# Kernel optimization log

Measured on AMD Instinct MI355X. Metric: run time of the kernel, lower is better.

Reference implementation:

```python
import jax, jax.numpy as jnp
import numpy as np

T, IN, OUT, R = 8192, 4096, 4096, 64


def setup_inputs() -> dict:
    key = jax.random.key(0)
    ks = jax.random.split(key, 7)
    # signed int4 values in [-8, 8) for activations and (unpacked) weights
    quant_x = jax.random.randint(ks[0], (T, IN), -8, 8, dtype=jnp.int32)
    weight_q = jax.random.randint(ks[1], (OUT, IN), -8, 8, dtype=jnp.int32)
    # positive per-token / per-channel symmetric-quant scales
    scale_x = jax.random.uniform(ks[2], (T,), dtype=jnp.float32) * 0.01 + 1e-4
    weight_scales = jax.random.uniform(ks[3], (OUT,), dtype=jnp.float32) * 0.01 + 1e-4
    outlier_x = jax.random.normal(ks[4], (T, R), dtype=jnp.float32)
    w_outlier = jax.random.normal(ks[5], (OUT, R), dtype=jnp.float32)
    bias = jax.random.normal(ks[6], (OUT,), dtype=jnp.float32)
    return {"quant_x": quant_x, "weight_q": weight_q, "scale_x": scale_x,
            "weight_scales": weight_scales, "outlier_x": outlier_x,
            "w_outlier": w_outlier, "bias": bias}


def reference(quant_x, weight_q, scale_x, weight_scales, outlier_x, w_outlier, bias):
    acc = jnp.matmul(quant_x, weight_q.T)
    # sym_dequant: per-row activation scale * per-column weight scale
    x_out = acc.astype(jnp.float32) * scale_x[:, None] * weight_scales[None, :]
    # outlier low-rank addmm + bias epilogue
    x_out = x_out + jnp.matmul(outlier_x, w_outlier.T) + bias
    return x_out
```

## Files before the change

kernel.cpp:

```cpp
#include <hip/hip_runtime.h>

#define T_DIM 8192
#define IN_DIM 4096
#define OUT_DIM 4096
#define R_DIM 64
#define NKP 32

typedef int i32x4 __attribute__((ext_vector_type(4)));
typedef float f32x4 __attribute__((ext_vector_type(4)));
typedef _Float16 f16x8 __attribute__((ext_vector_type(8)));

__device__ __forceinline__ int pack4(int4 v) {
  return (v.x & 255) | ((v.y & 255) << 8) | ((v.z & 255) << 16) | ((unsigned)v.w << 24);
}

__device__ __forceinline__ void gload16(const void* g, void* l) {
  __builtin_amdgcn_global_load_lds(
      (const __attribute__((address_space(1))) void*)(unsigned long long)g,
      (__attribute__((address_space(3))) void*)(unsigned)(unsigned long long)l,
      16, 0, 0);
}

__device__ __forceinline__ i32x4 unp(int x, int y) {
  i32x4 r;
  r[0] = x & 0x0F0F0F0F;
  r[1] = (x >> 4) & 0x0F0F0F0F;
  r[2] = y & 0x0F0F0F0F;
  r[3] = (y >> 4) & 0x0F0F0F0F;
  return r;
}

__device__ __forceinline__ unsigned pb(int a, int b) {
  return (unsigned)(a + 8) | ((unsigned)(b + 8) << 4);
}

__global__ __launch_bounds__(256)
void cvt_pack_kernel(const int* __restrict__ qx, const int* __restrict__ wq,
                     char* __restrict__ pk, int* __restrict__ SS) {
  const int wave = blockIdx.x * 4 + (threadIdx.x >> 6);
  const int l = threadIdx.x & 63;
  const int nw = gridDim.x * 4;
  for (int r = wave; r < T_DIM + OUT_DIM; r += nw) {
    const int* src = (r < T_DIM) ? (qx + (size_t)r * IN_DIM)
                                 : (wq + (size_t)(r - T_DIM) * IN_DIM);
    const int4* src4 = (const int4*)src;
    char* dst = pk + (size_t)r * 2048;
    const int rx = (r >> 1) & 3;
    int s = 0;
#pragma unroll
    for (int i = 0; i < 4; ++i) {
      const int q = i * 64 + l;
      const int kt = q >> 2, g = q & 3;
      int4 s0 = src4[q * 4 + 0], s1 = src4[q * 4 + 1];
      int4 s2 = src4[q * 4 + 2], s3 = src4[q * 4 + 3];
      s += s0.x + s0.y + s0.z + s0.w + s1.x + s1.y + s1.z + s1.w +
           s2.x + s2.y + s2.z + s2.w + s3.x + s3.y + s3.z + s3.w;
      unsigned dw0 = pb(s0.x, s0.y) | (pb(s0.z, s0.w) << 8) |
                     (pb(s1.x, s1.y) << 16) | (pb(s1.z, s1.w) << 24);
      unsigned dw1 = pb(s2.x, s2.y) | (pb(s2.z, s2.w) << 8) |
                     (pb(s3.x, s3.y) << 16) | (pb(s3.z, s3.w) << 24);
      const int off = (kt >> 1) * 64 + ((g ^ rx) << 4) + (kt & 1) * 8;
      *(uint2*)(dst + off) = make_uint2(dw0, dw1);
    }
#pragma unroll
    for (int off = 1; off < 64; off <<= 1) s += __shfl_xor(s, off, 64);
    if (l == 0) SS[r] = s + 8 * IN_DIM;
  }
}

__global__ __launch_bounds__(256, 2)
void w4a4_gemm(const char* __restrict__ A8, const char* __restrict__ B8,
               const int* __restrict__ SS,
               const float* __restrict__ sx, const float* __restrict__ sw,
               const float* __restrict__ ox, const float* __restrict__ ow,
               const float* __restrict__ bias, float* __restrict__ out) {
  __shared__ __align__(16) char smem[49152];

  const int bid = blockIdx.x;
  const int xcd = bid & 7, c = bid >> 3;
  const int tn = (xcd & 3) * 8 + (c & 7);
  const int tm = (xcd >> 2) * 32 + (c >> 3);
  const int brow = tm * 128, bcol = tn * 128;

  const int t = threadIdx.x;
  const int w = t >> 6, l = t & 63;
  const int wr = w >> 1, wc = w & 1;
  const int l16 = l & 15, lk = l >> 4;

  const char* gA0 = A8 + (size_t)(brow + (t >> 2)) * 2048 + (t & 3) * 16;
  const char* gA1 = gA0 + (size_t)64 * 2048;
  const char* gB0 = B8 + (size_t)(bcol + (t >> 2)) * 2048 + (t & 3) * 16;
  const char* gB1 = gB0 + (size_t)64 * 2048;
  char* const dA0 = smem + t * 16;
  char* const dA1 = smem + 4096 + t * 16;
  char* const dB0 = smem + 8192 + t * 16;
  char* const dB1 = smem + 12288 + t * 16;

  const int Ra = wr * 64 + l16;
  const int Cb = wc * 64 + l16;
  const char* aR = smem + Ra * 64 + ((lk ^ ((Ra >> 1) & 3)) << 4);
  const char* bR = smem + 8192 + Cb * 64 + ((lk ^ ((Cb >> 1) & 3)) << 4);

  i32x4 acc[4][4];
#pragma unroll
  for (int m = 0; m < 4; ++m)
#pragma unroll
    for (int n = 0; n < 4; ++n) acc[m][n] = (i32x4){0, 0, 0, 0};

  auto stage = [&](int kp) {
    const int off = kp << 6;
    const int buf = (kp % 3) * 16384;
    gload16(gA0 + off, dA0 + buf);
    gload16(gA1 + off, dA1 + buf);
    gload16(gB0 + off, dB0 + buf);
    gload16(gB1 + off, dB1 + buf);
  };

  auto compute = [&](int kp) {
    const int buf = (kp % 3) * 16384;
    const char* sa = aR + buf;
    const char* sb = bR + buf;
    i32x4 ap[4], bp[4];
#pragma unroll
    for (int m = 0; m < 4; ++m) ap[m] = *(const i32x4*)(sa + m * 1024);
#pragma unroll
    for (int n = 0; n < 4; ++n) bp[n] = *(const i32x4*)(sb + n * 1024);
    i32x4 bv[4];
#pragma unroll
    for (int n = 0; n < 4; ++n) bv[n] = unp(bp[n][0], bp[n][1]);
    __builtin_amdgcn_s_setprio(1);
#pragma unroll
    for (int m = 0; m < 4; ++m) {
      i32x4 av = unp(ap[m][0], ap[m][1]);
      acc[m][0] = __builtin_amdgcn_mfma_i32_16x16x64_i8(av, bv[0], acc[m][0], 0, 0, 0);
      acc[m][1] = __builtin_amdgcn_mfma_i32_16x16x64_i8(av, bv[1], acc[m][1], 0, 0, 0);
      acc[m][2] = __builtin_amdgcn_mfma_i32_16x16x64_i8(av, bv[2], acc[m][2], 0, 0, 0);
      acc[m][3] = __builtin_amdgcn_mfma_i32_16x16x64_i8(av, bv[3], acc[m][3], 0, 0, 0);
    }
    __builtin_amdgcn_s_setprio(0);
#pragma unroll
    for (int n = 0; n < 4; ++n) bv[n] = unp(bp[n][2], bp[n][3]);
    __builtin_amdgcn_s_setprio(1);
#pragma unroll
    for (int m = 0; m < 4; ++m) {
      i32x4 av = unp(ap[m][2], ap[m][3]);
      acc[m][0] = __builtin_amdgcn_mfma_i32_16x16x64_i8(av, bv[0], acc[m][0], 0, 0, 0);
      acc[m][1] = __builtin_amdgcn_mfma_i32_16x16x64_i8(av, bv[1], acc[m][1], 0, 0, 0);
      acc[m][2] = __builtin_amdgcn_mfma_i32_16x16x64_i8(av, bv[2], acc[m][2], 0, 0, 0);
      acc[m][3] = __builtin_amdgcn_mfma_i32_16x16x64_i8(av, bv[3], acc[m][3], 0, 0, 0);
    }
    __builtin_amdgcn_s_setprio(0);
  };

#define VMBAR(N)                                          \
  asm volatile("s_waitcnt vmcnt(" #N ")" ::: "memory");   \
  __builtin_amdgcn_s_barrier();                           \
  __builtin_amdgcn_sched_barrier(0);

  stage(0); stage(1);
  for (int kp = 0; kp < NKP - 2; ++kp) {
    VMBAR(4);
    stage(kp + 2);
    compute(kp);
  }
  VMBAR(4);
  compute(NKP - 2);
  VMBAR(0);
  compute(NKP - 1);

  const int orow0 = brow + wr * 64 + (lk << 2);
  const int ocol0 = bcol + wc * 64 + l16;
  const int* SA = SS;
  const int* SB = SS + T_DIM;
  float swv[4], bvv[4];
  int cb[4];
#pragma unroll
  for (int n = 0; n < 4; ++n) {
    swv[n] = sw[ocol0 + n * 16];
    bvv[n] = bias[ocol0 + n * 16];
    cb[n] = -8 * SB[ocol0 + n * 16];
  }

  f32x4 facc[4][4];
#pragma unroll
  for (int m = 0; m < 4; ++m) {
#pragma unroll
    for (int r = 0; r < 4; ++r) {
      const int row = orow0 + m * 16 + r;
      const float sxv = sx[row];
      const int ca = 262144 - 8 * SA[row];
#pragma unroll
      for (int n = 0; n < 4; ++n)
        facc[m][n][r] = (float)(acc[m][n][r] + ca + cb[n]) * sxv * swv[n];
    }
  }

  __syncthreads();
#pragma unroll
  for (int j = 0; j < 4; ++j) {
    int q = j * 256 + t;
    int row = q >> 3, cd = q & 7, cs = cd ^ (row & 7);
    const float* ga = ox + (size_t)(brow + row) * R_DIM + cs * 8;
    float4 f0 = *(const float4*)ga, f1 = *(const float4*)(ga + 4);
    f16x8 h;
    h[0] = (_Float16)f0.x; h[1] = (_Float16)f0.y; h[2] = (_Float16)f0.z; h[3] = (_Float16)f0.w;
    h[4] = (_Float16)f1.x; h[5] = (_Float16)f1.y; h[6] = (_Float16)f1.z; h[7] = (_Float16)f1.w;
    *(f16x8*)(smem + row * 128 + cd * 16) = h;
    const float* gb = ow + (size_t)(bcol + row) * R_DIM + cs * 8;
    f0 = *(const float4*)gb; f1 = *(const float4*)(gb + 4);
    f16x8 g;
    g[0] = (_Float16)f0.x; g[1] = (_Float16)f0.y; g[2] = (_Float16)f0.z; g[3] = (_Float16)f0.w;
    g[4] = (_Float16)f1.x; g[5] = (_Float16)f1.y; g[6] = (_Float16)f1.z; g[7] = (_Float16)f1.w;
    *(f16x8*)(smem + 16384 + row * 128 + cd * 16) = g;
  }
  __syncthreads();

  const char* qa = smem + (wr * 64 + l16) * 128;
  const char* qb = smem + 16384 + (wc * 64 + l16) * 128;
  const int x7 = l16 & 7;
#pragma unroll
  for (int s = 0; s < 2; ++s) {
    const int ca2 = ((s * 4 + lk) ^ x7) << 4;
    f16x8 hb[4];
#pragma unroll
    for (int n = 0; n < 4; ++n) hb[n] = *(const f16x8*)(qb + n * 2048 + ca2);
#pragma unroll
    for (int m = 0; m < 4; ++m) {
      f16x8 ha = *(const f16x8*)(qa + m * 2048 + ca2);
#pragma unroll
      for (int n = 0; n < 4; ++n)
        facc[m][n] = __builtin_amdgcn_mfma_f32_16x16x32_f16(ha, hb[n], facc[m][n], 0, 0, 0);
    }
  }

#pragma unroll
  for (int m = 0; m < 4; ++m)
#pragma unroll
    for (int r = 0; r < 4; ++r) {
      float* po = out + (size_t)(orow0 + m * 16 + r) * OUT_DIM + ocol0;
#pragma unroll
      for (int n = 0; n < 4; ++n) po[n * 16] = facc[m][n][r] + bvv[n];
    }
}

__global__ __launch_bounds__(256)
void w4a4_gemm_fb(const int* __restrict__ A32, const int* __restrict__ B32,
                  const float* __restrict__ sx, const float* __restrict__ sw,
                  const float* __restrict__ ox, const float* __restrict__ ow,
                  const float* __restrict__ bias, float* __restrict__ out) {
  __shared__ __align__(16) unsigned char smem[32768];
  char* sA = (char*)smem;
  char* sB = (char*)smem + 8192;

  const int bid = blockIdx.x;
  const int swzb = (bid & 7) * 256 + (bid >> 3);
  const int tm = swzb >> 5, tn = swzb & 31;
  const int brow = tm * 128, bcol = tn * 128;

  const int t = threadIdx.x;
  const int l = t & 63;
  const int wr = (t >> 6) >> 1, wc = (t >> 6) & 1;
  const int l16 = l & 15, lk = l >> 4;

  i32x4 iacc[4][4];
#pragma unroll
  for (int m = 0; m < 4; ++m)
#pragma unroll
    for (int n = 0; n < 4; ++n) iacc[m][n] = (i32x4){0, 0, 0, 0};

  const int ar = t >> 2;
  const int ac = (t & 3) << 4;
  const int* hA0 = A32 + (size_t)(brow + ar) * IN_DIM + ac;
  const int* hA1 = hA0 + (size_t)64 * IN_DIM;
  const int* hB0 = B32 + (size_t)(bcol + ar) * IN_DIM + ac;
  const int* hB1 = hB0 + (size_t)64 * IN_DIM;

  const char* fragA = sA + (size_t)(wr * 64 + l16) * 64 + lk * 16;
  const char* fragB = sB + (size_t)(wc * 64 + l16) * 64 + lk * 16;

  for (int k0 = 0; k0 < IN_DIM; k0 += 64) {
    const int4* pA0 = (const int4*)(hA0 + k0);
    int4 r0 = {pack4(pA0[0]), pack4(pA0[1]), pack4(pA0[2]), pack4(pA0[3])};
    *(int4*)(sA + t * 16) = r0;
    const int4* pA1 = (const int4*)(hA1 + k0);
    int4 r1 = {pack4(pA1[0]), pack4(pA1[1]), pack4(pA1[2]), pack4(pA1[3])};
    *(int4*)(sA + 4096 + t * 16) = r1;
    const int4* pB0 = (const int4*)(hB0 + k0);
    int4 r2 = {pack4(pB0[0]), pack4(pB0[1]), pack4(pB0[2]), pack4(pB0[3])};
    *(int4*)(sB + t * 16) = r2;
    const int4* pB1 = (const int4*)(hB1 + k0);
    int4 r3 = {pack4(pB1[0]), pack4(pB1[1]), pack4(pB1[2]), pack4(pB1[3])};
    *(int4*)(sB + 4096 + t * 16) = r3;
    __syncthreads();
    i32x4 av[4], bv[4];
#pragma unroll
    for (int m = 0; m < 4; ++m) av[m] = *(const i32x4*)(fragA + m * 1024);
#pragma unroll
    for (int n = 0; n < 4; ++n) bv[n] = *(const i32x4*)(fragB + n * 1024);
#pragma unroll
    for (int m = 0; m < 4; ++m)
#pragma unroll
      for (int n = 0; n < 4; ++n)
        iacc[m][n] = __builtin_amdgcn_mfma_i32_16x16x64_i8(av[m], bv[n], iacc[m][n], 0, 0, 0);
    __syncthreads();
  }

  const int orow = brow + wr * 64 + lk * 4;
  const int ocol = bcol + wc * 64 + l16;
  float swv[4], bvv[4];
#pragma unroll
  for (int n = 0; n < 4; ++n) { swv[n] = sw[ocol + n * 16]; bvv[n] = bias[ocol + n * 16]; }

  f32x4 facc[4][4];
#pragma unroll
  for (int m = 0; m < 4; ++m)
#pragma unroll
    for (int r = 0; r < 4; ++r) {
      float sxv = sx[orow + m * 16 + r];
#pragma unroll
      for (int n = 0; n < 4; ++n) facc[m][n][r] = (float)iacc[m][n][r] * sxv * swv[n];
    }

  _Float16* oA = (_Float16*)smem;
  _Float16* oB = (_Float16*)(smem + 16384);
#pragma unroll
  for (int j = 0; j < 4; ++j) {
    int c = j * 256 + t;
    int rr2 = c >> 3, c8 = (c & 7) << 3;
    const float* gp = ox + (size_t)(brow + rr2) * R_DIM + c8;
    float4 f0 = *(const float4*)gp;
    float4 f1 = *(const float4*)(gp + 4);
    f16x8 h;
    h[0] = (_Float16)f0.x; h[1] = (_Float16)f0.y; h[2] = (_Float16)f0.z; h[3] = (_Float16)f0.w;
    h[4] = (_Float16)f1.x; h[5] = (_Float16)f1.y; h[6] = (_Float16)f1.z; h[7] = (_Float16)f1.w;
    *(f16x8*)((char*)oA + (size_t)c * 16) = h;
    const float* gq = ow + (size_t)(bcol + rr2) * R_DIM + c8;
    f0 = *(const float4*)gq; f1 = *(const float4*)(gq + 4);
    f16x8 g;
    g[0] = (_Float16)f0.x; g[1] = (_Float16)f0.y; g[2] = (_Float16)f0.z; g[3] = (_Float16)f0.w;
    g[4] = (_Float16)f1.x; g[5] = (_Float16)f1.y; g[6] = (_Float16)f1.z; g[7] = (_Float16)f1.w;
    *(f16x8*)((char*)oB + (size_t)c * 16) = g;
  }
  __syncthreads();

  const char* qa = (const char*)oA + (size_t)(wr * 64 + l16) * 128 + lk * 16;
  const char* qb = (const char*)oB + (size_t)(wc * 64 + l16) * 128 + lk * 16;
#pragma unroll
  for (int s = 0; s < 2; ++s) {
    f16x8 ha[4], hb[4];
#pragma unroll
    for (int m = 0; m < 4; ++m) ha[m] = *(const f16x8*)(qa + m * 2048 + s * 64);
#pragma unroll
    for (int n = 0; n < 4; ++n) hb[n] = *(const f16x8*)(qb + n * 2048 + s * 64);
#pragma unroll
    for (int m = 0; m < 4; ++m)
#pragma unroll
      for (int n = 0; n < 4; ++n)
        facc[m][n] = __builtin_amdgcn_mfma_f32_16x16x32_f16(ha[m], hb[n], facc[m][n], 0, 0, 0);
  }

#pragma unroll
  for (int m = 0; m < 4; ++m)
#pragma unroll
    for (int r = 0; r < 4; ++r) {
      float* po = out + (size_t)(orow + m * 16 + r) * OUT_DIM + ocol;
#pragma unroll
      for (int n = 0; n < 4; ++n) po[n * 16] = facc[m][n][r] + bvv[n];
    }
}

extern "C" void kernel_launch(void* const* d_in, const int* in_sizes, int n_in,
                              void* d_out, int out_size, void* d_ws, size_t ws_size,
                              hipStream_t stream) {
  const int*   qx   = (const int*)d_in[0];
  const int*   wq   = (const int*)d_in[1];
  const float* sx   = (const float*)d_in[2];
  const float* sw   = (const float*)d_in[3];
  const float* ox   = (const float*)d_in[4];
  const float* ow   = (const float*)d_in[5];
  const float* bias = (const float*)d_in[6];
  float* out = (float*)d_out;

  const size_t packedA = (size_t)T_DIM * 2048;
  const size_t packedB = (size_t)OUT_DIM * 2048;
  const size_t ssBytes = (size_t)(T_DIM + OUT_DIM) * 4;
  const size_t need = packedA + packedB + ssBytes;

  if (ws_size >= need) {
    char* pk = (char*)d_ws;
    int* SS = (int*)(pk + packedA + packedB);
    cvt_pack_kernel<<<768, 256, 0, stream>>>(qx, wq, pk, SS);
    w4a4_gemm<<<2048, 256, 0, stream>>>(pk, pk + packedA, SS, sx, sw, ox, ow, bias, out);
  } else {
    w4a4_gemm_fb<<<2048, 256, 0, stream>>>(qx, wq, sx, sw, ox, ow, bias, out);
  }
}
```

Measured before the change: 169.8 us.

## Deepen LDS pipeline to four buffers and register double-buffer fragment reads

Moves the shared-memory ring from three to four stages (64KB LDS) and adds register double-buffering, so the LDS reads for the next k-step are issued before the MFMAs of the current step. The aim is to hide LDS read latency behind matrix instructions and keep more global loads in flight. In exchange it uses more LDS and registers, which could hurt occupancy under the 2-blocks-per-CU launch bound, and the hand-written barrier ordering adds risk of races on buffer reuse.

```diff
diff --git a/kernel.cpp b/kernel.cpp
--- a/kernel.cpp
+++ b/kernel.cpp
@@ -74,7 +74,7 @@
                const float* __restrict__ sx, const float* __restrict__ sw,
                const float* __restrict__ ox, const float* __restrict__ ow,
                const float* __restrict__ bias, float* __restrict__ out) {
-  __shared__ __align__(16) char smem[49152];
+  __shared__ __align__(16) char smem[65536];
 
   const int bid = blockIdx.x;
   const int xcd = bid & 7, c = bid >> 3;
@@ -109,64 +109,88 @@
 
   auto stage = [&](int kp) {
     const int off = kp << 6;
-    const int buf = (kp % 3) * 16384;
+    const int buf = (kp & 3) << 14;
     gload16(gA0 + off, dA0 + buf);
     gload16(gA1 + off, dA1 + buf);
     gload16(gB0 + off, dB0 + buf);
     gload16(gB1 + off, dB1 + buf);
   };
 
-  auto compute = [&](int kp) {
-    const int buf = (kp % 3) * 16384;
-    const char* sa = aR + buf;
-    const char* sb = bR + buf;
-    i32x4 ap[4], bp[4];
-#pragma unroll
-    for (int m = 0; m < 4; ++m) ap[m] = *(const i32x4*)(sa + m * 1024);
-#pragma unroll
-    for (int n = 0; n < 4; ++n) bp[n] = *(const i32x4*)(sb + n * 1024);
-    i32x4 bv[4];
-#pragma unroll
-    for (int n = 0; n < 4; ++n) bv[n] = unp(bp[n][0], bp[n][1]);
-    __builtin_amdgcn_s_setprio(1);
-#pragma unroll
-    for (int m = 0; m < 4; ++m) {
-      i32x4 av = unp(ap[m][0], ap[m][1]);
-      acc[m][0] = __builtin_amdgcn_mfma_i32_16x16x64_i8(av, bv[0], acc[m][0], 0, 0, 0);
-      acc[m][1] = __builtin_amdgcn_mfma_i32_16x16x64_i8(av, bv[1], acc[m][1], 0, 0, 0);
-      acc[m][2] = __builtin_amdgcn_mfma_i32_16x16x64_i8(av, bv[2], acc[m][2], 0, 0, 0);
-      acc[m][3] = __builtin_amdgcn_mfma_i32_16x16x64_i8(av, bv[3], acc[m][3], 0, 0, 0);
-    }
-    __builtin_amdgcn_s_setprio(0);
-#pragma unroll
-    for (int n = 0; n < 4; ++n) bv[n] = unp(bp[n][2], bp[n][3]);
-    __builtin_amdgcn_s_setprio(1);
-#pragma unroll
-    for (int m = 0; m < 4; ++m) {
-      i32x4 av = unp(ap[m][2], ap[m][3]);
-      acc[m][0] = __builtin_amdgcn_mfma_i32_16x16x64_i8(av, bv[0], acc[m][0], 0, 0, 0);
-      acc[m][1] = __builtin_amdgcn_mfma_i32_16x16x64_i8(av, bv[1], acc[m][1], 0, 0, 0);
-      acc[m][2] = __builtin_amdgcn_mfma_i32_16x16x64_i8(av, bv[2], acc[m][2], 0, 0, 0);
-      acc[m][3] = __builtin_amdgcn_mfma_i32_16x16x64_i8(av, bv[3], acc[m][3], 0, 0, 0);
-    }
-    __builtin_amdgcn_s_setprio(0);
-  };
+  i32x4 apA[4], bpA[4], apB[4], bpB[4];
+
+#define PREFETCH(AP, BP, BUFN)                                         \
+  {                                                                    \
+    const char* sa_ = aR + (BUFN);                                     \
+    const char* sb_ = bR + (BUFN);                                     \
+    _Pragma("unroll")                                                  \
+    for (int m_ = 0; m_ < 4; ++m_) AP[m_] = *(const i32x4*)(sa_ + m_ * 1024); \
+    _Pragma("unroll")                                                  \
+    for (int n_ = 0; n_ < 4; ++n_) BP[n_] = *(const i32x4*)(sb_ + n_ * 1024); \
+  }
+
+#define MFMAS(AP, BP)                                                  \
+  {                                                                    \
+    i32x4 bv0 = unp(BP[0][0], BP[0][1]);                               \
+    i32x4 bv1 = unp(BP[1][0], BP[1][1]);                               \
+    i32x4 bv2 = unp(BP[2][0], BP[2][1]);                               \
+    i32x4 bv3 = unp(BP[3][0], BP[3][1]);                               \
+    __builtin_amdgcn_s_setprio(1);                                     \
+    _Pragma("unroll")                                                  \
+    for (int m_ = 0; m_ < 4; ++m_) {                                   \
+      i32x4 av = unp(AP[m_][0], AP[m_][1]);                            \
+      acc[m_][0] = __builtin_amdgcn_mfma_i32_16x16x64_i8(av, bv0, acc[m_][0], 0, 0, 0); \
+      acc[m_][1] = __builtin_amdgcn_mfma_i32_16x16x64_i8(av, bv1, acc[m_][1], 0, 0, 0); \
+      acc[m_][2] = __builtin_amdgcn_mfma_i32_16x16x64_i8(av, bv2, acc[m_][2], 0, 0, 0); \
+      acc[m_][3] = __builtin_amdgcn_mfma_i32_16x16x64_i8(av, bv3, acc[m_][3], 0, 0, 0); \
+    }                                                                  \
+    __builtin_amdgcn_s_setprio(0);                                     \
+    bv0 = unp(BP[0][2], BP[0][3]);                                     \
+    bv1 = unp(BP[1][2], BP[1][3]);                                     \
+    bv2 = unp(BP[2][2], BP[2][3]);                                     \
+    bv3 = unp(BP[3][2], BP[3][3]);                                     \
+    __builtin_amdgcn_s_setprio(1);                                     \
+    _Pragma("unroll")                                                  \
+    for (int m_ = 0; m_ < 4; ++m_) {                                   \
+      i32x4 av = unp(AP[m_][2], AP[m_][3]);                            \
+      acc[m_][0] = __builtin_amdgcn_mfma_i32_16x16x64_i8(av, bv0, acc[m_][0], 0, 0, 0); \
+      acc[m_][1] = __builtin_amdgcn_mfma_i32_16x16x64_i8(av, bv1, acc[m_][1], 0, 0, 0); \
+      acc[m_][2] = __builtin_amdgcn_mfma_i32_16x16x64_i8(av, bv2, acc[m_][2], 0, 0, 0); \
+      acc[m_][3] = __builtin_amdgcn_mfma_i32_16x16x64_i8(av, bv3, acc[m_][3], 0, 0, 0); \
+    }                                                                  \
+    __builtin_amdgcn_s_setprio(0);                                     \
+  }
 
 #define VMBAR(N)                                          \
   asm volatile("s_waitcnt vmcnt(" #N ")" ::: "memory");   \
   __builtin_amdgcn_s_barrier();                           \
   __builtin_amdgcn_sched_barrier(0);
 
-  stage(0); stage(1);
-  for (int kp = 0; kp < NKP - 2; ++kp) {
+  stage(0); stage(1); stage(2);
+  VMBAR(4);
+  PREFETCH(apA, bpA, 0);
+
+  for (int kp = 0; kp < 28; kp += 2) {
+    stage(kp + 3);
+    PREFETCH(apB, bpB, ((kp + 1) & 3) << 14);
+    MFMAS(apA, bpA);
     VMBAR(4);
-    stage(kp + 2);
-    compute(kp);
-  }
+    stage(kp + 4);
+    PREFETCH(apA, bpA, ((kp + 2) & 3) << 14);
+    MFMAS(apB, bpB);
+    VMBAR(4);
+  }
+  stage(31);
+  PREFETCH(apB, bpB, (29 & 3) << 14);
+  MFMAS(apA, bpA);
   VMBAR(4);
-  compute(NKP - 2);
-  VMBAR(0);
-  compute(NKP - 1);
+  PREFETCH(apA, bpA, (30 & 3) << 14);
+  MFMAS(apB, bpB);
+  asm volatile("s_waitcnt vmcnt(0)" ::: "memory");
+  __builtin_amdgcn_s_barrier();
+  __builtin_amdgcn_sched_barrier(0);
+  PREFETCH(apB, bpB, (31 & 3) << 14);
+  MFMAS(apA, bpA);
+  MFMAS(apB, bpB);
 
   const int orow0 = brow + wr * 64 + (lk << 2);
   const int ocol0 = bcol + wc * 64 + l16;
```

Result: slower. 174.1 us (+2.5%).
